# Kernel optimization log

Hardware: AMD Instinct MI355X
Metric: run time of the kernel (lower is better)

## Reference

```python
import jax, jax.numpy as jnp
import numpy as np

N_NODES = 50000


def setup_inputs() -> dict:
    key = jax.random.key(0)
    k1, k2, k3 = jax.random.split(key, 3)
    x = jax.random.normal(k1, (N_NODES, 256), dtype=jnp.float32)
    edge_index = jax.random.randint(k2, (2, 1600000), 0, N_NODES, dtype=jnp.int64)
    W = jax.random.normal(k3, (256, 256), dtype=jnp.float32) / np.sqrt(256.0)
    b = jnp.zeros((256,), dtype=jnp.float32)
    return {"x": x, "edge_index": edge_index, "W": W, "b": b}


def reference(x, edge_index, W, b):
    # PyG GCNConv: add self-loops, symmetric normalization, linear, aggregate, bias; then ReLU.
    n = x.shape[0]
    self_loops = jnp.arange(n, dtype=edge_index.dtype)
    src = jnp.concatenate([edge_index[0], self_loops])  # [E+N]
    dst = jnp.concatenate([edge_index[1], self_loops])  # [E+N]

    # degree from incoming edges (incl. self loops)
    deg = jax.ops.segment_sum(jnp.ones_like(dst, dtype=x.dtype), dst, num_segments=n)
    dinv = jnp.where(deg > 0, jax.lax.rsqrt(deg), 0.0)
    norm = dinv[src] * dinv[dst]  # [E+N]

    xw = x @ W  # [N, out] linear first (GCNConv transforms then propagates)
    msgs = xw[src] * norm[:, None]  # gather + edge-normalize
    agg = jax.ops.segment_sum(msgs, dst, num_segments=n)  # scatter-add
    return jax.nn.relu(agg + b)
```

## Files before the change

kernel.cpp:

```cpp
#include <hip/hip_runtime.h>
#include <hip/hip_bf16.h>


#define FEATS 256
#define MAXBUCK 200
#define P1_CAP 64
#define BCAP 10240

typedef __bf16 bf16x8 __attribute__((ext_vector_type(8)));
typedef float f32x4 __attribute__((ext_vector_type(4)));

__device__ __forceinline__ unsigned short f2bf(float f) {
  unsigned u = __float_as_uint(f);
  u += 0x7fffu + ((u >> 16) & 1u);
  return (unsigned short)(u >> 16);
}
__device__ __forceinline__ float bflo(unsigned u) { return __uint_as_float(u << 16); }
__device__ __forceinline__ float bfhi(unsigned u) { return __uint_as_float(u & 0xFFFF0000u); }


__global__ __launch_bounds__(512) void init_misc(int* __restrict__ gcursor, int nbuck,
                                                 int* __restrict__ xwp_i, int npad, int n) {
  const int t = threadIdx.x;
  if (t < nbuck) gcursor[t] = 0;
  const int j = t - 256;
  if (j >= 0 && j < 128) {
    const int s = j >> 4, w = j & 15;
    xwp_i[((size_t)s * npad + n) * 16 + w] = 0;
  }
}


__global__ __launch_bounds__(1024) void pass1_bin(const int* __restrict__ src,
                                                  const int* __restrict__ dst,
                                                  int E, int nbuck,
                                                  int* __restrict__ gcursor,
                                                  unsigned* __restrict__ temp) {
  __shared__ unsigned lbuf[MAXBUCK * P1_CAP];
  __shared__ int lcnt[MAXBUCK];
  __shared__ int lbase[MAXBUCK];
  const int tid = threadIdx.x;
  for (int i = tid; i < nbuck; i += 1024) lcnt[i] = 0;
  __syncthreads();

  const int e0 = blockIdx.x * 4096;
  #pragma unroll
  for (int i = 0; i < 4; ++i) {
    int e = e0 + i * 1024 + tid;
    if (e < E) {
      unsigned d = (unsigned)dst[e];
      unsigned p = (d << 16) | (unsigned)src[e];
      int b = (int)(d >> 8);
      int pos = atomicAdd(&lcnt[b], 1);
      if (pos < P1_CAP) {
        lbuf[b * P1_CAP + pos] = p;
      } else {
        int gp = atomicAdd(&gcursor[b], 1);
        temp[(size_t)b * BCAP + gp] = p;
      }
    }
  }
  __syncthreads();
  if (tid < nbuck) {
    int c = lcnt[tid]; if (c > P1_CAP) c = P1_CAP;
    lcnt[tid] = c;
    lbase[tid] = atomicAdd(&gcursor[tid], c);
  }
  __syncthreads();
  for (int i = tid; i < nbuck * P1_CAP; i += 1024) {
    int b = i >> 6, j = i & (P1_CAP - 1);
    if (j < lcnt[b]) temp[(size_t)b * BCAP + lbase[b] + j] = lbuf[i];
  }
}

__global__ __launch_bounds__(256) void scan_buckets(const int* __restrict__ gcursor,
                                                    int* __restrict__ bbase,
                                                    int* __restrict__ row_ptr,
                                                    int nbuck, int n) {
  __shared__ int tmp[256];
  int t = threadIdx.x;
  int v = (t < nbuck) ? min(gcursor[t], BCAP) : 0;
  tmp[t] = v;
  __syncthreads();
  #pragma unroll
  for (int off = 1; off < 256; off <<= 1) {
    int x = (t >= off) ? tmp[t - off] : 0;
    __syncthreads();
    tmp[t] += x;
    __syncthreads();
  }
  if (t < nbuck) bbase[t] = tmp[t] - v;
  if (t == 0) row_ptr[n] = tmp[255];
}

__global__ __launch_bounds__(1024) void pass2_csr(const unsigned* __restrict__ temp,
                                                  const int* __restrict__ gcursor,
                                                  const int* __restrict__ bbase,
                                                  unsigned short* __restrict__ csr16,
                                                  int* __restrict__ row_ptr,
                                                  float* __restrict__ dinv, int n) {
  __shared__ unsigned ebuf[BCAP];
  __shared__ unsigned short sorted[BCAP];
  __shared__ int hist[256], scn[256], sexcl[256], ofs[256];
  const int b = blockIdx.x;
  const int tid = threadIdx.x;
  int cnt = gcursor[b]; if (cnt > BCAP) cnt = BCAP;
  const int base = bbase[b];
  const unsigned* tp = temp + (size_t)b * BCAP;

  if (tid < 256) { hist[tid] = 0; ofs[tid] = 0; }
  for (int i = tid; i < cnt; i += 1024) ebuf[i] = tp[i];
  __syncthreads();
  for (int i = tid; i < cnt; i += 1024) atomicAdd(&hist[(ebuf[i] >> 16) & 255], 1);
  __syncthreads();

  if (tid < 256) scn[tid] = hist[tid];
  __syncthreads();
  #pragma unroll
  for (int off = 1; off < 256; off <<= 1) {
    int x = 0;
    if (tid < 256 && tid >= off) x = scn[tid - off];
    __syncthreads();
    if (tid < 256) scn[tid] += x;
    __syncthreads();
  }
  if (tid < 256) {
    int v = hist[tid];
    int excl = scn[tid] - v;
    sexcl[tid] = excl;
    int node = (b << 8) + tid;
    if (node < n) {
      row_ptr[node] = base + excl;
      dinv[node] = rsqrtf((float)(v + 1));
    }
  }
  __syncthreads();

  for (int i = tid; i < cnt; i += 1024) {
    unsigned e = ebuf[i];
    int dl = (int)((e >> 16) & 255);
    int pos = sexcl[dl] + atomicAdd(&ofs[dl], 1);
    sorted[pos] = (unsigned short)(e & 0xFFFFu);
  }
  __syncthreads();
  for (int i = tid; i < cnt; i += 1024) csr16[base + i] = sorted[i];
}


__global__ __launch_bounds__(256) void wt_build(const float* __restrict__ W,
                                                unsigned short* __restrict__ Wt) {
  int k = blockIdx.x;
  int nn = threadIdx.x;
  Wt[nn * FEATS + k] = f2bf(W[k * FEATS + nn]);
}


__global__ __launch_bounds__(256, 2) void gemm_mfma(const float* __restrict__ x,
                                                    const unsigned short* __restrict__ Wt,
                                                    const float* __restrict__ dinv,
                                                    unsigned short* __restrict__ xwp,
                                                    int M, int npad) {
  __shared__ bf16x8 A_lds[32 * 64];
  const int wv   = (int)(threadIdx.x >> 6);
  const int lane = (int)(threadIdx.x & 63);
  const int lm   = lane & 15;
  const int quad = lane >> 4;
  const int m0   = (int)blockIdx.x * 64;

  bf16x8 Bfrag[4][8];
  #pragma unroll
  for (int ct = 0; ct < 4; ++ct) {
    const unsigned short* wrow = Wt + (size_t)(wv * 64 + ct * 16 + lm) * FEATS + quad * 8;
    #pragma unroll
    for (int kc = 0; kc < 8; ++kc)
      Bfrag[ct][kc] = *(const bf16x8*)(wrow + kc * 32);
  }

  {
    int arow = m0 + wv * 16 + lm; if (arow >= M) arow = M - 1;
    const float* xrow = x + (size_t)arow * FEATS + quad * 8;
    #pragma unroll
    for (int kc = 0; kc < 8; ++kc) {
      const float4 f0 = *(const float4*)(xrow + kc * 32);
      const float4 f1 = *(const float4*)(xrow + kc * 32 + 4);
      union { bf16x8 v; unsigned short u[8]; } a;
      a.u[0] = f2bf(f0.x); a.u[1] = f2bf(f0.y); a.u[2] = f2bf(f0.z); a.u[3] = f2bf(f0.w);
      a.u[4] = f2bf(f1.x); a.u[5] = f2bf(f1.y); a.u[6] = f2bf(f1.z); a.u[7] = f2bf(f1.w);
      A_lds[(wv * 8 + kc) * 64 + lane] = a.v;
    }
  }
  __syncthreads();

  #pragma unroll
  for (int sub = 0; sub < 4; ++sub) {
    bf16x8 Af[8];
    #pragma unroll
    for (int kc = 0; kc < 8; ++kc) Af[kc] = A_lds[(sub * 8 + kc) * 64 + lane];

    f32x4 acc[4];
    #pragma unroll
    for (int ct = 0; ct < 4; ++ct) acc[ct] = (f32x4){0.f, 0.f, 0.f, 0.f};

    #pragma unroll
    for (int kc = 0; kc < 8; ++kc) {
      #pragma unroll
      for (int ct = 0; ct < 4; ++ct)
        acc[ct] = __builtin_amdgcn_mfma_f32_16x16x32_bf16(Af[kc], Bfrag[ct][kc], acc[ct], 0, 0, 0);
    }

    #pragma unroll
    for (int r = 0; r < 4; ++r) {
      const int row = m0 + sub * 16 + quad * 4 + r;
      if (row < M) {
        const float dd = dinv[row];
        #pragma unroll
        for (int ct = 0; ct < 4; ++ct) {
          const int c = wv * 64 + ct * 16 + lm;
          const int sl = c >> 5, off = c & 31;
          xwp[((size_t)sl * npad + row) * 32 + off] = f2bf(acc[ct][r] * dd);
        }
      }
    }
  }
}


__global__ __launch_bounds__(256) void aggregate(const unsigned short* __restrict__ xwp,
                                                 const float* __restrict__ dinv,
                                                 const int* __restrict__ row_ptr,
                                                 const unsigned short* __restrict__ csr16,
                                                 const float* __restrict__ bias,
                                                 float* __restrict__ out,
                                                 int n, int npad, int nbps, int sl0) {
  const int sl   = sl0 + (int)(blockIdx.x / nbps);
  const int nb   = (int)(blockIdx.x % nbps);
  const int wv   = (int)(threadIdx.x >> 6);
  const int lane = (int)(threadIdx.x & 63);
  const int eg   = lane >> 3;
  const int cl   = lane & 7;
  const int node = nb * 32 + wv * 8 + eg;
  const bool valid = node < n;
  const int nodec = valid ? node : n;

  const unsigned short* xs = xwp + (size_t)sl * npad * 32 + cl * 4;

  uint2 v0 = *(const uint2*)(xs + (size_t)nodec * 32);
  float4 acc;
  acc.x = bflo(v0.x); acc.y = bfhi(v0.x); acc.z = bflo(v0.y); acc.w = bfhi(v0.y);

  const int beg = valid ? row_ptr[node] : 0;
  const int end = valid ? row_ptr[node + 1] : 0;
  const int deg = end - beg;
  int mdeg = deg;
  #pragma unroll
  for (int st = 8; st < 64; st <<= 1) mdeg = max(mdeg, __shfl_xor(mdeg, st));

  for (int t = 0; t < mdeg; t += 8) {
    int sj[8];
    uint2 vv[8];
    #pragma unroll
    for (int j = 0; j < 8; ++j) {
      const int it = t + j;
      const int a = (it < deg) ? beg + it : 0;
      sj[j] = (it < deg) ? (int)csr16[a] : n;
    }
    #pragma unroll
    for (int j = 0; j < 8; ++j)
      vv[j] = *(const uint2*)(xs + (size_t)sj[j] * 32);
    #pragma unroll
    for (int j = 0; j < 8; ++j) {
      acc.x += bflo(vv[j].x); acc.y += bfhi(vv[j].x);
      acc.z += bflo(vv[j].y); acc.w += bfhi(vv[j].y);
    }
  }

  if (valid) {
    const float dd = dinv[node];
    const float4 bb = *(const float4*)(bias + sl * 32 + cl * 4);
    f32x4 o;
    o.x = fmaxf(fmaf(acc.x, dd, bb.x), 0.f);
    o.y = fmaxf(fmaf(acc.y, dd, bb.y), 0.f);
    o.z = fmaxf(fmaf(acc.z, dd, bb.z), 0.f);
    o.w = fmaxf(fmaf(acc.w, dd, bb.w), 0.f);
    __builtin_nontemporal_store(o, (f32x4*)(out + (size_t)node * 256 + sl * 32 + cl * 4));
  }
}


extern "C" void kernel_launch(void* const* d_in, const int* in_sizes, int n_in,
                              void* d_out, int out_size, void* d_ws, size_t ws_size,
                              hipStream_t stream) {
  const float* x  = (const float*)d_in[0];
  const int*   ei = (const int*)d_in[1];
  const float* W  = (const float*)d_in[2];
  const float* b  = (const float*)d_in[3];

  const int n = in_sizes[0] / FEATS;
  const int E = in_sizes[1] / 2;
  const int* src = ei;
  const int* dst = ei + E;
  const int nbuck = (n + 255) >> 8;
  const int npad = n + 1;

  char* ws = (char*)d_ws;
  size_t o0 = 0;
  unsigned short* xwp   = (unsigned short*)(ws + o0); o0 += (size_t)npad * 512;
  unsigned short* Wt    = (unsigned short*)(ws + o0); o0 += 131072;
  float*          dinv  = (float*)(ws + o0);          o0 += 200064;
  int*            row_ptr = (int*)(ws + o0);          o0 += 200064;
  unsigned short* csr16 = (unsigned short*)(ws + o0); o0 += 3200000;
  int*            gcursor = (int*)(ws + o0);          o0 += 1024;
  int*            bbase   = (int*)(ws + o0);          o0 += 1024;
  unsigned*       temp    = (unsigned*)(ws + o0);     o0 += (size_t)nbuck * BCAP * 4;

  hipLaunchKernelGGL(init_misc, dim3(1), dim3(512), 0, stream, gcursor, nbuck, (int*)xwp, npad, n);
  hipLaunchKernelGGL(wt_build, dim3(256), dim3(256), 0, stream, W, Wt);

  const int g_p1 = (E + 4095) / 4096;
  hipLaunchKernelGGL(pass1_bin, dim3(g_p1), dim3(1024), 0, stream, src, dst, E, nbuck, gcursor, temp);
  hipLaunchKernelGGL(scan_buckets, dim3(1), dim3(256), 0, stream, gcursor, bbase, row_ptr, nbuck, n);
  hipLaunchKernelGGL(pass2_csr, dim3(nbuck), dim3(1024), 0, stream, temp, gcursor, bbase,
                     csr16, row_ptr, dinv, n);

  hipLaunchKernelGGL(gemm_mfma, dim3((n + 63) / 64), dim3(256), 0, stream, x, Wt, dinv, xwp, n, npad);

  const int nbps = (n + 31) / 32;
  hipLaunchKernelGGL(aggregate, dim3(nbps * 4), dim3(256), 0, stream,
                     xwp, dinv, row_ptr, csr16, b, (float*)d_out, n, npad, nbps, 0);
  hipLaunchKernelGGL(aggregate, dim3(nbps * 4), dim3(256), 0, stream,
                     xwp, dinv, row_ptr, csr16, b, (float*)d_out, n, npad, nbps, 4);
}
```

Measured before the change: 260.9 us.

## Stage neighbor indices in LDS and loop all feature slices per block

The aggregate kernel now handles 64 nodes per block and stages each node's first 64 neighbor indices in shared memory once. It then loops over all 8 feature slices inside the block instead of launching two kernels, each with a grid covering 4 slices. Each lane gathers 16-byte (8 bf16) chunks instead of 8-byte chunks, and 16 neighbors are in flight per step. This removes the repeated row_ptr and csr16 reads for every slice and one kernel launch. In exchange the grid shrinks, per-block work grows with serial slice loops, which hurts slice-level parallelism, and neighbors beyond 64 fall back to global index loads.

New measurement: 294.8 us. 1.13x slower.

```diff
diff --git a/kernel.cpp b/kernel.cpp
--- a/kernel.cpp
+++ b/kernel.cpp
@@ -6,6 +6,8 @@
 #define MAXBUCK 200
 #define P1_CAP 64
 #define BCAP 10240
+#define AGG_CAP 64
+#define AGG_STR 72
 
 typedef __bf16 bf16x8 __attribute__((ext_vector_type(8)));
 typedef float f32x4 __attribute__((ext_vector_type(4)));
@@ -231,58 +233,99 @@
                                                  const unsigned short* __restrict__ csr16,
                                                  const float* __restrict__ bias,
                                                  float* __restrict__ out,
-                                                 int n, int npad, int nbps, int sl0) {
-  const int sl   = sl0 + (int)(blockIdx.x / nbps);
-  const int nb   = (int)(blockIdx.x % nbps);
+                                                 int n, int npad) {
+  __shared__ __align__(16) unsigned short idx_lds[64 * AGG_STR];
   const int wv   = (int)(threadIdx.x >> 6);
   const int lane = (int)(threadIdx.x & 63);
-  const int eg   = lane >> 3;
-  const int cl   = lane & 7;
-  const int node = nb * 32 + wv * 8 + eg;
+  const int eg   = lane >> 2;
+  const int cl   = lane & 3;
+  const int nb0  = (int)blockIdx.x * 64;
+  const int node = nb0 + wv * 16 + eg;
   const bool valid = node < n;
   const int nodec = valid ? node : n;
 
-  const unsigned short* xs = xwp + (size_t)sl * npad * 32 + cl * 4;
-
-  uint2 v0 = *(const uint2*)(xs + (size_t)nodec * 32);
-  float4 acc;
-  acc.x = bflo(v0.x); acc.y = bfhi(v0.x); acc.z = bflo(v0.y); acc.w = bfhi(v0.y);
+  #pragma unroll 1
+  for (int ln = 0; ln < 16; ++ln) {
+    const int nd = nb0 + wv * 16 + ln;
+    unsigned short v = (unsigned short)n;
+    if (nd < n) {
+      const int b0 = row_ptr[nd];
+      const int d  = row_ptr[nd + 1] - b0;
+      if (lane < d) v = csr16[b0 + lane];
+    }
+    idx_lds[(wv * 16 + ln) * AGG_STR + lane] = v;
+  }
 
   const int beg = valid ? row_ptr[node] : 0;
-  const int end = valid ? row_ptr[node + 1] : 0;
-  const int deg = end - beg;
+  const int deg = valid ? row_ptr[node + 1] - beg : 0;
   int mdeg = deg;
   #pragma unroll
-  for (int st = 8; st < 64; st <<= 1) mdeg = max(mdeg, __shfl_xor(mdeg, st));
-
-  for (int t = 0; t < mdeg; t += 8) {
-    int sj[8];
-    uint2 vv[8];
-    #pragma unroll
-    for (int j = 0; j < 8; ++j) {
-      const int it = t + j;
-      const int a = (it < deg) ? beg + it : 0;
-      sj[j] = (it < deg) ? (int)csr16[a] : n;
-    }
-    #pragma unroll
-    for (int j = 0; j < 8; ++j)
-      vv[j] = *(const uint2*)(xs + (size_t)sj[j] * 32);
-    #pragma unroll
-    for (int j = 0; j < 8; ++j) {
-      acc.x += bflo(vv[j].x); acc.y += bfhi(vv[j].x);
-      acc.z += bflo(vv[j].y); acc.w += bfhi(vv[j].y);
-    }
-  }
-
-  if (valid) {
-    const float dd = dinv[node];
-    const float4 bb = *(const float4*)(bias + sl * 32 + cl * 4);
-    f32x4 o;
-    o.x = fmaxf(fmaf(acc.x, dd, bb.x), 0.f);
-    o.y = fmaxf(fmaf(acc.y, dd, bb.y), 0.f);
-    o.z = fmaxf(fmaf(acc.z, dd, bb.z), 0.f);
-    o.w = fmaxf(fmaf(acc.w, dd, bb.w), 0.f);
-    __builtin_nontemporal_store(o, (f32x4*)(out + (size_t)node * 256 + sl * 32 + cl * 4));
+  for (int st = 4; st < 64; st <<= 1) mdeg = max(mdeg, __shfl_xor(mdeg, st));
+  const int lim = min(mdeg, AGG_CAP);
+
+  const float dd = valid ? dinv[node] : 0.f;
+  const uint4* lq = (const uint4*)(idx_lds + (wv * 16 + eg) * AGG_STR);
+
+  for (int sl = 0; sl < 8; ++sl) {
+    const unsigned short* xs = xwp + (size_t)sl * npad * 32 + cl * 8;
+    uint4 v = *(const uint4*)(xs + ((size_t)nodec << 5));
+    float a0 = bflo(v.x), a1 = bfhi(v.x), a2 = bflo(v.y), a3 = bfhi(v.y);
+    float a4 = bflo(v.z), a5 = bfhi(v.z), a6 = bflo(v.w), a7 = bfhi(v.w);
+
+    for (int j0 = 0; j0 < lim; j0 += 16) {
+      const uint4 q0 = lq[(j0 >> 3)];
+      const uint4 q1 = lq[(j0 >> 3) + 1];
+      const unsigned qq[8] = {q0.x, q0.y, q0.z, q0.w, q1.x, q1.y, q1.z, q1.w};
+      uint4 vv[16];
+      #pragma unroll
+      for (int k = 0; k < 8; ++k) {
+        vv[2 * k]     = *(const uint4*)(xs + ((size_t)(qq[k] & 0xFFFFu) << 5));
+        vv[2 * k + 1] = *(const uint4*)(xs + ((size_t)(qq[k] >> 16) << 5));
+      }
+      #pragma unroll
+      for (int k = 0; k < 16; ++k) {
+        a0 += bflo(vv[k].x); a1 += bfhi(vv[k].x);
+        a2 += bflo(vv[k].y); a3 += bfhi(vv[k].y);
+        a4 += bflo(vv[k].z); a5 += bfhi(vv[k].z);
+        a6 += bflo(vv[k].w); a7 += bfhi(vv[k].w);
+      }
+    }
+    if (mdeg > AGG_CAP) {
+      for (int j0 = AGG_CAP; j0 < mdeg; j0 += 8) {
+        int sj[8]; uint4 vv[8];
+        #pragma unroll
+        for (int k = 0; k < 8; ++k) {
+          const int j = j0 + k;
+          sj[k] = (j < deg) ? (int)csr16[beg + j] : n;
+        }
+        #pragma unroll
+        for (int k = 0; k < 8; ++k) vv[k] = *(const uint4*)(xs + ((size_t)sj[k] << 5));
+        #pragma unroll
+        for (int k = 0; k < 8; ++k) {
+          a0 += bflo(vv[k].x); a1 += bfhi(vv[k].x);
+          a2 += bflo(vv[k].y); a3 += bfhi(vv[k].y);
+          a4 += bflo(vv[k].z); a5 += bfhi(vv[k].z);
+          a6 += bflo(vv[k].w); a7 += bfhi(vv[k].w);
+        }
+      }
+    }
+
+    if (valid) {
+      const float4 b0 = *(const float4*)(bias + sl * 32 + cl * 8);
+      const float4 b1 = *(const float4*)(bias + sl * 32 + cl * 8 + 4);
+      f32x4 o0, o1;
+      o0.x = fmaxf(fmaf(a0, dd, b0.x), 0.f);
+      o0.y = fmaxf(fmaf(a1, dd, b0.y), 0.f);
+      o0.z = fmaxf(fmaf(a2, dd, b0.z), 0.f);
+      o0.w = fmaxf(fmaf(a3, dd, b0.w), 0.f);
+      o1.x = fmaxf(fmaf(a4, dd, b1.x), 0.f);
+      o1.y = fmaxf(fmaf(a5, dd, b1.y), 0.f);
+      o1.z = fmaxf(fmaf(a6, dd, b1.z), 0.f);
+      o1.w = fmaxf(fmaf(a7, dd, b1.w), 0.f);
+      float* op = out + (size_t)node * 256 + sl * 32 + cl * 8;
+      __builtin_nontemporal_store(o0, (f32x4*)op);
+      __builtin_nontemporal_store(o1, (f32x4*)(op + 4));
+    }
   }
 }
 
@@ -324,9 +367,6 @@
 
   hipLaunchKernelGGL(gemm_mfma, dim3((n + 63) / 64), dim3(256), 0, stream, x, Wt, dinv, xwp, n, npad);
 
-  const int nbps = (n + 31) / 32;
-  hipLaunchKernelGGL(aggregate, dim3(nbps * 4), dim3(256), 0, stream,
-                     xwp, dinv, row_ptr, csr16, b, (float*)d_out, n, npad, nbps, 0);
-  hipLaunchKernelGGL(aggregate, dim3(nbps * 4), dim3(256), 0, stream,
-                     xwp, dinv, row_ptr, csr16, b, (float*)d_out, n, npad, nbps, 4);
-}
+  hipLaunchKernelGGL(aggregate, dim3((n + 63) / 64), dim3(256), 0, stream,
+                     xwp, dinv, row_ptr, csr16, b, (float*)d_out, n, npad);
+}
```
